# Performance work log

Measured on AMD Instinct MI355X. Metric: run time of the kernel, lower is better.

The kernel has to match this reference:

```python
import jax, jax.numpy as jnp
import numpy as np

DIM = 192
NUM_HEADS = 6
KSZ = 7
MLP_RATIO = 4.0
LEVELS = 8
EPS = 1e-5


def layernorm(x, w, b):
    mu = jnp.mean(x, axis=-1, keepdims=True)
    var = jnp.mean(jnp.square(x - mu), axis=-1, keepdims=True)
    return (x - mu) * jax.lax.rsqrt(var + EPS) * w + b


def na2d(x, qkv_w, qkv_b, proj_w, proj_b, rpb):
    # Neighborhood attention 2D with relative position bias (NATTEN semantics:
    # window of KSZ x KSZ keys per query, clamped to stay inside the image).
    B, H, W, C = x.shape
    nh, hd = NUM_HEADS, C // NUM_HEADS
    scale = hd ** -0.5
    qkv = (x @ qkv_w.T + qkv_b).reshape(B, H, W, 3, nh, hd)
    q = qkv[..., 0, :, :] * scale  # [B,H,W,nh,hd]
    k = qkv[..., 1, :, :]
    v = qkv[..., 2, :, :]

    si = jnp.clip(jnp.arange(H) - KSZ // 2, 0, H - KSZ)
    idx_i = si[:, None] + jnp.arange(KSZ)  # [H,KSZ] row indices of each window
    sj = jnp.clip(jnp.arange(W) - KSZ // 2, 0, W - KSZ)
    idx_j = sj[:, None] + jnp.arange(KSZ)  # [W,KSZ]

    def gather_win(t):  # [B,H,W,nh,hd] -> [B,H,KSZ,W,KSZ,nh,hd]
        t = jnp.take(t, idx_i.reshape(-1), axis=1).reshape(B, H, KSZ, W, nh, hd)
        t = jnp.take(t, idx_j.reshape(-1), axis=3).reshape(B, H, KSZ, W, KSZ, nh, hd)
        return t

    kw = gather_win(k)
    vw = gather_win(v)

    # scores over the KSZ x KSZ neighborhood
    scores = jnp.einsum('bxynd,bxiyjnd->bxynij', q, kw)  # [B,H,W,nh,KSZ,KSZ]

    # relative position bias: rpb is [nh, 2K-1, 2K-1]
    rel_i = idx_i - jnp.arange(H)[:, None] + (KSZ - 1)  # [H,KSZ] in [0,2K-2]
    rel_j = idx_j - jnp.arange(W)[:, None] + (KSZ - 1)  # [W,KSZ]
    bias = rpb[:, rel_i][:, :, :, rel_j]  # [nh,H,KSZ,W,KSZ]
    scores = scores + bias.transpose(1, 3, 0, 2, 4)[None]

    attn = jax.nn.softmax(scores.reshape(B, H, W, nh, KSZ * KSZ), axis=-1)
    attn = attn.reshape(B, H, W, nh, KSZ, KSZ)
    out = jnp.einsum('bxynij,bxiyjnd->bxynd', attn, vw).reshape(B, H, W, C)
    return out @ proj_w.T + proj_b


def setup_inputs() -> dict:
    key = jax.random.key(0)
    ks = jax.random.split(key, 8)
    C = DIM
    hidden = int(C * MLP_RATIO)
    init = lambda k, shape: (jax.random.normal(k, shape, dtype=jnp.float32) * 0.02)
    return {
        'x': jax.random.normal(ks[0], (1, 128, 128, C), dtype=jnp.float32),
        'qkv_w': init(ks[1], (3 * C, C)),
        'qkv_b': jnp.zeros((3 * C,), jnp.float32),
        'proj_w': init(ks[2], (C, C)),
        'proj_b': jnp.zeros((C,), jnp.float32),
        'rpb': init(ks[3], (NUM_HEADS, 2 * KSZ - 1, 2 * KSZ - 1)),
        'ln1_w': jnp.ones((C,), jnp.float32),
        'ln1_b': jnp.zeros((C,), jnp.float32),
        'ln2_w': jnp.ones((C,), jnp.float32),
        'ln2_b': jnp.zeros((C,), jnp.float32),
        'fc1_w': init(ks[4], (hidden, C)),
        'fc1_b': jnp.zeros((hidden,), jnp.float32),
        'fc2_w': init(ks[5], (C, hidden)),
        'fc2_b': jnp.zeros((C,), jnp.float32),
        'gamma1': jnp.ones((LEVELS, C), jnp.float32),
        'gamma2': jnp.ones((LEVELS, C), jnp.float32),
        'quality': 4,
    }


def reference(x, qkv_w, qkv_b, proj_w, proj_b, rpb, ln1_w, ln1_b, ln2_w, ln2_b,
              fc1_w, fc1_b, fc2_w, fc2_b, gamma1, gamma2, quality):
    # eval-mode quality gating; quality is an integer so l = quality % 1 == 0
    s = int(quality) - 1
    g1 = jnp.abs(gamma1[s])
    g2 = jnp.abs(gamma2[s])

    shortcut = x
    h = layernorm(x, ln1_w, ln1_b)
    a = na2d(h, qkv_w, qkv_b, proj_w, proj_b, rpb)
    x = shortcut + g1 * a
    h2 = layernorm(x, ln2_w, ln2_b)
    m = jax.nn.gelu(h2 @ fc1_w.T + fc1_b, approximate=False) @ fc2_w.T + fc2_b
    x = x + g2 * m
    return x
```

## Files before the change

### kernel.cpp

```cpp
#include <hip/hip_runtime.h>
#include <hip/hip_bf16.h>
#include <math.h>

#define DIM 192
#define NHD 6
#define HD 32
#define KSZ 7
#define HID 768
#define IMH 128
#define IMW 128
#define NPIX (IMH*IMW)
#define WIN 14
#define KPAD 40

typedef __attribute__((ext_vector_type(8))) short short8;
typedef __attribute__((ext_vector_type(4))) float f32x4;

__global__ __launch_bounds__(256) void cvt_ln1(
    const float* __restrict__ qw, const float* __restrict__ pw,
    const float* __restrict__ f1, const float* __restrict__ f2,
    __hip_bfloat16* dq, __hip_bfloat16* dp, __hip_bfloat16* df1, __hip_bfloat16* df2,
    const float* __restrict__ x, const float* __restrict__ w, const float* __restrict__ b,
    __hip_bfloat16* __restrict__ hout)
{
    int blk = blockIdx.x, t = threadIdx.x;
    if (blk < 1728) {
        const float* s; __hip_bfloat16* d; int idx;
        if (blk < 432)       { s = qw; d = dq;  idx = blk * 256 + t; }
        else if (blk < 576)  { s = pw; d = dp;  idx = (blk - 432) * 256 + t; }
        else if (blk < 1152) { s = f1; d = df1; idx = (blk - 576) * 256 + t; }
        else                 { s = f2; d = df2; idx = (blk - 1152) * 256 + t; }
        d[idx] = __float2bfloat16(s[idx]);
        return;
    }
    int wid  = ((blk - 1728) * 256 + t) >> 6;
    int lane = t & 63;
    const float* xp = x + (size_t)wid * DIM;
    float v0 = xp[lane], v1 = xp[lane + 64], v2 = xp[lane + 128];
    float s = v0 + v1 + v2;
    #pragma unroll
    for (int off = 32; off > 0; off >>= 1) s += __shfl_down(s, off);
    float mu = __shfl(s, 0) * (1.0f / DIM);
    float d0 = v0 - mu, d1 = v1 - mu, d2 = v2 - mu;
    float q = d0*d0 + d1*d1 + d2*d2;
    #pragma unroll
    for (int off = 32; off > 0; off >>= 1) q += __shfl_down(q, off);
    float rstd = rsqrtf(__shfl(q, 0) * (1.0f / DIM) + 1e-5f);
    __hip_bfloat16* op = hout + (size_t)wid * DIM;
    op[lane]       = __float2bfloat16(d0 * rstd * w[lane]       + b[lane]);
    op[lane + 64]  = __float2bfloat16(d1 * rstd * w[lane + 64]  + b[lane + 64]);
    op[lane + 128] = __float2bfloat16(d2 * rstd * w[lane + 128] + b[lane + 128]);
}

__device__ __forceinline__ void gl_lds16(const void* g, void* l) {
    __builtin_amdgcn_global_load_lds(
        (const __attribute__((address_space(1))) void*)g,
        (__attribute__((address_space(3))) void*)l, 16, 0, 0);
}

template<int mode>
__global__ __launch_bounds__(256) void gemm_k192(
    const __hip_bfloat16* __restrict__ A, const __hip_bfloat16* __restrict__ W,
    const float* __restrict__ bias,
    float* outf, __hip_bfloat16* outb, __hip_bfloat16* kb, __hip_bfloat16* vb, int N)
{
    __shared__ __hip_bfloat16 As[128 * 192];
    __shared__ __hip_bfloat16 Bs[64 * 192];
    int tid = threadIdx.x;
    int wave = tid >> 6, lane = tid & 63;
    int m0 = blockIdx.x * 128, n0 = blockIdx.y * 64;
    int q = lane >> 4, col = lane & 15;
    int wm = (wave >> 1) * 64, wn = (wave & 1) * 32;

    const __hip_bfloat16* Ab = A + (size_t)m0 * 192;
    #pragma unroll
    for (int i = 0; i < 12; i++) {
        int c = i * 256 + tid;
        int r = c / 24, kc = c - r * 24;
        int g = kc ^ (r & 7);
        gl_lds16(Ab + r * 192 + g * 8, (char*)As + (i * 256 + wave * 64) * 16);
    }
    const __hip_bfloat16* Wb = W + (size_t)n0 * 192;
    #pragma unroll
    for (int i = 0; i < 6; i++) {
        int c = i * 256 + tid;
        int r = c / 24, kc = c - r * 24;
        int g = kc ^ (r & 7);
        gl_lds16(Wb + r * 192 + g * 8, (char*)Bs + (i * 256 + wave * 64) * 16);
    }
    __syncthreads();

    f32x4 acc[4][2] = {};
    #pragma unroll
    for (int ks = 0; ks < 6; ks++) {
        short8 af[4], bf[2];
        #pragma unroll
        for (int mi = 0; mi < 4; mi++) {
            int r = wm + mi * 16 + col;
            af[mi] = *(const short8*)&As[r * 192 + (((ks * 4 + q) ^ (r & 7)) * 8)];
        }
        #pragma unroll
        for (int ni = 0; ni < 2; ni++) {
            int r = wn + ni * 16 + col;
            bf[ni] = *(const short8*)&Bs[r * 192 + (((ks * 4 + q) ^ (r & 7)) * 8)];
        }
        #pragma unroll
        for (int mi = 0; mi < 4; mi++)
            #pragma unroll
            for (int ni = 0; ni < 2; ni++)
                acc[mi][ni] = __builtin_amdgcn_mfma_f32_16x16x32_bf16(
                    af[mi], bf[ni], acc[mi][ni], 0, 0, 0);
    }

    #pragma unroll
    for (int mi = 0; mi < 4; mi++) {
        #pragma unroll
        for (int r = 0; r < 4; r++) {
            int m = m0 + wm + mi * 16 + q * 4 + r;
            #pragma unroll
            for (int ni = 0; ni < 2; ni++) {
                int n = n0 + wn + ni * 16 + col;
                float v = acc[mi][ni][r] + bias[n];
                if (mode == 0) {
                    int h18 = n >> 5;
                    int sel = h18 / 6;
                    int head = h18 - sel * 6;
                    size_t idx = ((size_t)head * NPIX + m) * 32 + (n & 31);
                    if (sel == 0)      outf[idx] = v * 0.17677669529663687f;
                    else if (sel == 1) kb[idx] = __float2bfloat16(v);
                    else               vb[idx] = __float2bfloat16(v);
                } else {
                    float u = 0.7978845608f * (v + 0.044715f * v * v * v);
                    float t = 1.f - 2.f / (__expf(2.f * u) + 1.f);
                    v = 0.5f * v * (1.f + t);
                    outb[(size_t)m * N + n] = __float2bfloat16(v);
                }
            }
        }
    }
}

__global__ __launch_bounds__(256) void proj_ln(
    const __hip_bfloat16* __restrict__ A, const __hip_bfloat16* __restrict__ W,
    const float* __restrict__ bias,
    float* outf, __hip_bfloat16* hb, const float* __restrict__ resid,
    const float* __restrict__ gamma, const int* __restrict__ quality,
    const float* __restrict__ lnw, const float* __restrict__ lnb)
{
    __shared__ __hip_bfloat16 As[64 * 192];
    __shared__ __hip_bfloat16 Bs[192 * 192];
    int tid = threadIdx.x;
    int wave = tid >> 6, lane = tid & 63;
    int q = lane >> 4, col = lane & 15;
    int m0 = blockIdx.x * 64;

    const __hip_bfloat16* Ab = A + (size_t)m0 * 192;
    #pragma unroll
    for (int i = 0; i < 6; i++) {
        int c = i * 256 + tid;
        int r = c / 24, kc = c - r * 24;
        int g = kc ^ (r & 7);
        gl_lds16(Ab + r * 192 + g * 8, (char*)As + (i * 256 + wave * 64) * 16);
    }
    #pragma unroll
    for (int i = 0; i < 18; i++) {
        int c = i * 256 + tid;
        int r = c / 24, kc = c - r * 24;
        int g = kc ^ (r & 7);
        gl_lds16(W + r * 192 + g * 8, (char*)Bs + (i * 256 + wave * 64) * 16);
    }
    __syncthreads();

    f32x4 acc[12] = {};
    #pragma unroll
    for (int ks = 0; ks < 6; ks++) {
        int rA = wave * 16 + col;
        short8 af = *(const short8*)&As[rA * 192 + (((ks * 4 + q) ^ (rA & 7)) * 8)];
        #pragma unroll
        for (int f = 0; f < 12; f++) {
            int rB = f * 16 + col;
            short8 bf = *(const short8*)&Bs[rB * 192 + (((ks * 4 + q) ^ (rB & 7)) * 8)];
            acc[f] = __builtin_amdgcn_mfma_f32_16x16x32_bf16(af, bf, acc[f], 0, 0, 0);
        }
    }

    int s = quality[0] - 1;
    float v[12][4];
    #pragma unroll
    for (int f = 0; f < 12; f++) {
        int n = f * 16 + col;
        float bi = bias[n];
        float g = fabsf(gamma[s * DIM + n]);
        #pragma unroll
        for (int r = 0; r < 4; r++) {
            int m = m0 + wave * 16 + q * 4 + r;
            v[f][r] = resid[(size_t)m * DIM + n] + g * (acc[f][r] + bi);
            outf[(size_t)m * DIM + n] = v[f][r];
        }
    }
    float sm[4] = {}, sq[4] = {};
    #pragma unroll
    for (int f = 0; f < 12; f++)
        #pragma unroll
        for (int r = 0; r < 4; r++) { sm[r] += v[f][r]; sq[r] += v[f][r] * v[f][r]; }
    #pragma unroll
    for (int off = 1; off <= 8; off <<= 1) {
        #pragma unroll
        for (int r = 0; r < 4; r++) {
            sm[r] += __shfl_xor(sm[r], off);
            sq[r] += __shfl_xor(sq[r], off);
        }
    }
    float mu[4], rstd[4];
    #pragma unroll
    for (int r = 0; r < 4; r++) {
        mu[r] = sm[r] * (1.0f / DIM);
        float var = sq[r] * (1.0f / DIM) - mu[r] * mu[r];
        rstd[r] = rsqrtf(var + 1e-5f);
    }
    #pragma unroll
    for (int f = 0; f < 12; f++) {
        int n = f * 16 + col;
        float lw = lnw[n], lb = lnb[n];
        #pragma unroll
        for (int r = 0; r < 4; r++) {
            int m = m0 + wave * 16 + q * 4 + r;
            hb[(size_t)m * DIM + n] = __float2bfloat16((v[f][r] - mu[r]) * rstd[r] * lw + lb);
        }
    }
}

__global__ __launch_bounds__(256) void fc2_gemm(
    const __hip_bfloat16* __restrict__ A, const __hip_bfloat16* __restrict__ W,
    const float* __restrict__ bias,
    float* outf, const float* __restrict__ resid,
    const float* __restrict__ gamma, const int* __restrict__ quality)
{
    __shared__ __hip_bfloat16 As[64 * 192];
    __shared__ __hip_bfloat16 Bs[64 * 192];
    int tid = threadIdx.x;
    int wave = tid >> 6, lane = tid & 63;
    int q = lane >> 4, col = lane & 15;
    int m0 = blockIdx.x * 64, n0 = blockIdx.y * 64;
    int wm = (wave >> 1) * 32, wn = (wave & 1) * 32;

    f32x4 acc[2][2] = {};
    for (int k0 = 0; k0 < HID; k0 += 192) {
        #pragma unroll
        for (int i = 0; i < 6; i++) {
            int c = i * 256 + tid;
            int r = c / 24, kc = c - r * 24;
            int g = kc ^ (r & 7);
            gl_lds16(A + (size_t)(m0 + r) * HID + k0 + g * 8,
                     (char*)As + (i * 256 + wave * 64) * 16);
        }
        #pragma unroll
        for (int i = 0; i < 6; i++) {
            int c = i * 256 + tid;
            int r = c / 24, kc = c - r * 24;
            int g = kc ^ (r & 7);
            gl_lds16(W + (size_t)(n0 + r) * HID + k0 + g * 8,
                     (char*)Bs + (i * 256 + wave * 64) * 16);
        }
        __syncthreads();
        #pragma unroll
        for (int ks = 0; ks < 6; ks++) {
            short8 af[2], bf[2];
            #pragma unroll
            for (int mi = 0; mi < 2; mi++) {
                int r = wm + mi * 16 + col;
                af[mi] = *(const short8*)&As[r * 192 + (((ks * 4 + q) ^ (r & 7)) * 8)];
            }
            #pragma unroll
            for (int ni = 0; ni < 2; ni++) {
                int r = wn + ni * 16 + col;
                bf[ni] = *(const short8*)&Bs[r * 192 + (((ks * 4 + q) ^ (r & 7)) * 8)];
            }
            #pragma unroll
            for (int mi = 0; mi < 2; mi++)
                #pragma unroll
                for (int ni = 0; ni < 2; ni++)
                    acc[mi][ni] = __builtin_amdgcn_mfma_f32_16x16x32_bf16(
                        af[mi], bf[ni], acc[mi][ni], 0, 0, 0);
        }
        __syncthreads();
    }

    int s = quality[0] - 1;
    #pragma unroll
    for (int mi = 0; mi < 2; mi++) {
        #pragma unroll
        for (int r = 0; r < 4; r++) {
            int m = m0 + wm + mi * 16 + q * 4 + r;
            #pragma unroll
            for (int ni = 0; ni < 2; ni++) {
                int n = n0 + wn + ni * 16 + col;
                float g = fabsf(gamma[s * DIM + n]);
                outf[(size_t)m * DIM + n] =
                    resid[(size_t)m * DIM + n] + g * (acc[mi][ni][r] + bias[n]);
            }
        }
    }
}

__device__ __forceinline__ void unpack8(const __hip_bfloat16* ptr, float* f) {
    short8 s8 = *(const short8*)ptr;
    union { short8 v; unsigned u[4]; } c; c.v = s8;
    #pragma unroll
    for (int w = 0; w < 4; w++) {
        f[2*w]   = __uint_as_float(c.u[w] << 16);
        f[2*w+1] = __uint_as_float(c.u[w] & 0xffff0000u);
    }
}

__global__ __launch_bounds__(256, 4) void attn_kernel3(
    const float* __restrict__ qbuf, const __hip_bfloat16* __restrict__ kbuf,
    const __hip_bfloat16* __restrict__ vbuf, const float* __restrict__ rpb,
    __hip_bfloat16* __restrict__ out)
{
    __shared__ __hip_bfloat16 Ks[WIN * WIN * KPAD];
    __shared__ __hip_bfloat16 Vs[WIN * WIN * KPAD];
    __shared__ float rpbs[169];

    int head = blockIdx.y;
    int tile = blockIdx.x;
    int ti0 = (tile >> 4) * 8;
    int tj0 = (tile & 15) * 8;
    int wi0 = ti0 - 3; wi0 = wi0 < 0 ? 0 : (wi0 > IMH - WIN ? IMH - WIN : wi0);
    int wj0 = tj0 - 3; wj0 = wj0 < 0 ? 0 : (wj0 > IMW - WIN ? IMW - WIN : wj0);

    int tid = threadIdx.x;
    const size_t hbase = (size_t)head * NPIX;

    for (int c = tid; c < 784; c += 256) {
        int i = c / 56, part = c - i * 56;
        int n = i * WIN + (part >> 2);
        int dp = part & 3;
        size_t goff = (hbase + (size_t)(wi0 + i) * IMW + wj0) * 32 + part * 8;
        short8 kk = *(const short8*)(kbuf + goff);
        short8 vv = *(const short8*)(vbuf + goff);
        *(short8*)&Ks[n * KPAD + dp * 8] = kk;
        *(short8*)&Vs[n * KPAD + dp * 8] = vv;
    }
    if (tid < 169) rpbs[tid] = rpb[head * 169 + tid];

    int p   = tid >> 2;
    int sub = tid & 3;
    int pi = ti0 + (p >> 3), pj = tj0 + (p & 7);
    int si = pi - 3; si = si < 0 ? 0 : (si > IMH - KSZ ? IMH - KSZ : si);
    int sj = pj - 3; sj = sj < 0 ? 0 : (sj > IMW - KSZ ? IMW - KSZ : sj);
    int bi = si - wi0, bj = sj - wj0;

    const float4* qp = (const float4*)(qbuf + (hbase + (size_t)(pi * IMW + pj)) * 32 + sub * 8);
    float4 q0 = qp[0], q1 = qp[1];
    float q[8] = {q0.x, q0.y, q0.z, q0.w, q1.x, q1.y, q1.z, q1.w};

    __syncthreads();

    float m = -1e30f, l = 0.f;
    float acc[8] = {};
    #pragma unroll
    for (int ki = 0; ki < KSZ; ki++) {
        int rbase = (bi + ki) * WIN + bj;
        const float* rb = &rpbs[(si + ki - pi + 6) * 13 + (sj - pj + 6)];
        float s7[KSZ];
        #pragma unroll
        for (int kj = 0; kj < KSZ; kj++) {
            float kf[8];
            unpack8(&Ks[(rbase + kj) * KPAD + sub * 8], kf);
            float d = q[0]*kf[0] + q[1]*kf[1] + q[2]*kf[2] + q[3]*kf[3]
                    + q[4]*kf[4] + q[5]*kf[5] + q[6]*kf[6] + q[7]*kf[7];
            d += __shfl_xor(d, 1);
            d += __shfl_xor(d, 2);
            s7[kj] = d + rb[kj];
        }
        float rmax = s7[0];
        #pragma unroll
        for (int kj = 1; kj < KSZ; kj++) rmax = fmaxf(rmax, s7[kj]);
        float mn = fmaxf(m, rmax);
        float co = __expf(m - mn);
        l *= co;
        #pragma unroll
        for (int e = 0; e < 8; e++) acc[e] *= co;
        #pragma unroll
        for (int kj = 0; kj < KSZ; kj++) {
            float pw = __expf(s7[kj] - mn);
            l += pw;
            float vf[8];
            unpack8(&Vs[(rbase + kj) * KPAD + sub * 8], vf);
            #pragma unroll
            for (int e = 0; e < 8; e++) acc[e] += pw * vf[e];
        }
        m = mn;
    }
    float rl = 1.f / l;
    __hip_bfloat16* op = out + (size_t)(pi * IMW + pj) * DIM + head * HD + sub * 8;
    #pragma unroll
    for (int e = 0; e < 8; e++) op[e] = __float2bfloat16(acc[e] * rl);
}

extern "C" void kernel_launch(void* const* d_in, const int* in_sizes, int n_in,
                              void* d_out, int out_size, void* d_ws, size_t ws_size,
                              hipStream_t stream)
{
    const float* x      = (const float*)d_in[0];
    const float* qkv_w  = (const float*)d_in[1];
    const float* qkv_b  = (const float*)d_in[2];
    const float* proj_w = (const float*)d_in[3];
    const float* proj_b = (const float*)d_in[4];
    const float* rpb    = (const float*)d_in[5];
    const float* ln1_w  = (const float*)d_in[6];
    const float* ln1_b  = (const float*)d_in[7];
    const float* ln2_w  = (const float*)d_in[8];
    const float* ln2_b  = (const float*)d_in[9];
    const float* fc1_w  = (const float*)d_in[10];
    const float* fc1_b  = (const float*)d_in[11];
    const float* fc2_w  = (const float*)d_in[12];
    const float* fc2_b  = (const float*)d_in[13];
    const float* gamma1 = (const float*)d_in[14];
    const float* gamma2 = (const float*)d_in[15];
    const int*   quality= (const int*)d_in[16];
    float* out = (float*)d_out;

    char* ws = (char*)d_ws;
    float*          qbuf   = (float*)ws;
    __hip_bfloat16* kbuf   = (__hip_bfloat16*)(ws + 12582912);
    __hip_bfloat16* vbuf   = (__hip_bfloat16*)(ws + 18874368);
    __hip_bfloat16* m1     = (__hip_bfloat16*)ws;
    __hip_bfloat16* h      = (__hip_bfloat16*)(ws + 37748736);
    __hip_bfloat16* attn_b = (__hip_bfloat16*)(ws + 44040192);
    __hip_bfloat16* wq     = (__hip_bfloat16*)(ws + 50331648);
    __hip_bfloat16* wp     = (__hip_bfloat16*)(ws + 50552832);
    __hip_bfloat16* wf1    = (__hip_bfloat16*)(ws + 50626560);
    __hip_bfloat16* wf2    = (__hip_bfloat16*)(ws + 50921472);

    cvt_ln1<<<1728 + NPIX / 4, 256, 0, stream>>>(
        qkv_w, proj_w, fc1_w, fc2_w, wq, wp, wf1, wf2, x, ln1_w, ln1_b, h);
    gemm_k192<0><<<dim3(NPIX / 128, 9), 256, 0, stream>>>(
        h, wq, qkv_b, qbuf, nullptr, kbuf, vbuf, 576);
    attn_kernel3<<<dim3(256, NHD), 256, 0, stream>>>(qbuf, kbuf, vbuf, rpb, attn_b);
    proj_ln<<<NPIX / 64, 256, 0, stream>>>(
        attn_b, wp, proj_b, out, h, x, gamma1, quality, ln2_w, ln2_b);
    gemm_k192<1><<<dim3(NPIX / 128, 12), 256, 0, stream>>>(
        h, wf1, fc1_b, nullptr, m1, nullptr, nullptr, HID);
    fc2_gemm<<<dim3(NPIX / 64, 3), 256, 0, stream>>>(
        m1, wf2, fc2_b, out, out, gamma2, quality);
}
```

Before: 182.5 us.

## Fuse fc1+GELU and fc2 into one MLP kernel keeping hidden activations in LDS

Replaces the separate fc1 GEMM (writing the 768-wide bf16 hidden tensor to global memory) and the fc2 GEMM with a single kernel. Each 64-row block loops over eight 96-wide hidden chunks: it computes fc1 plus GELU into shared memory, then immediately accumulates the fc2 contribution. fc2 weights are pre-permuted into chunked layout during conversion. This removes the hidden-activation round trip through HBM and one launch, at the cost of large LDS use (~100KB, low occupancy), 256 blocks only, and no overlap of chunk loads with compute.

```diff
diff --git a/kernel.cpp b/kernel.cpp
--- a/kernel.cpp
+++ b/kernel.cpp
@@ -25,12 +25,14 @@
 {
     int blk = blockIdx.x, t = threadIdx.x;
     if (blk < 1728) {
-        const float* s; __hip_bfloat16* d; int idx;
-        if (blk < 432)       { s = qw; d = dq;  idx = blk * 256 + t; }
-        else if (blk < 576)  { s = pw; d = dp;  idx = (blk - 432) * 256 + t; }
-        else if (blk < 1152) { s = f1; d = df1; idx = (blk - 576) * 256 + t; }
-        else                 { s = f2; d = df2; idx = (blk - 1152) * 256 + t; }
-        d[idx] = __float2bfloat16(s[idx]);
+        if (blk < 432)       { int i = blk * 256 + t; dq[i] = __float2bfloat16(qw[i]); }
+        else if (blk < 576)  { int i = (blk - 432) * 256 + t; dp[i] = __float2bfloat16(pw[i]); }
+        else if (blk < 1152) { int i = (blk - 576) * 256 + t; df1[i] = __float2bfloat16(f1[i]); }
+        else {
+            int i = (blk - 1152) * 256 + t;
+            int n = i / 768, k = i - n * 768;
+            df2[(k / 96) * 24576 + n * 128 + (k % 96)] = __float2bfloat16(f2[i]);
+        }
         return;
     }
     int wid  = ((blk - 1728) * 256 + t) >> 6;
@@ -121,20 +123,13 @@
             for (int ni = 0; ni < 2; ni++) {
                 int n = n0 + wn + ni * 16 + col;
                 float v = acc[mi][ni][r] + bias[n];
-                if (mode == 0) {
-                    int h18 = n >> 5;
-                    int sel = h18 / 6;
-                    int head = h18 - sel * 6;
-                    size_t idx = ((size_t)head * NPIX + m) * 32 + (n & 31);
-                    if (sel == 0)      outf[idx] = v * 0.17677669529663687f;
-                    else if (sel == 1) kb[idx] = __float2bfloat16(v);
-                    else               vb[idx] = __float2bfloat16(v);
-                } else {
-                    float u = 0.7978845608f * (v + 0.044715f * v * v * v);
-                    float t = 1.f - 2.f / (__expf(2.f * u) + 1.f);
-                    v = 0.5f * v * (1.f + t);
-                    outb[(size_t)m * N + n] = __float2bfloat16(v);
-                }
+                int h18 = n >> 5;
+                int sel = h18 / 6;
+                int head = h18 - sel * 6;
+                size_t idx = ((size_t)head * NPIX + m) * 32 + (n & 31);
+                if (sel == 0)      outf[idx] = v * 0.17677669529663687f;
+                else if (sel == 1) kb[idx] = __float2bfloat16(v);
+                else               vb[idx] = __float2bfloat16(v);
             }
         }
     }
@@ -230,75 +225,99 @@
     }
 }
 
-__global__ __launch_bounds__(256) void fc2_gemm(
-    const __hip_bfloat16* __restrict__ A, const __hip_bfloat16* __restrict__ W,
-    const float* __restrict__ bias,
-    float* outf, const float* __restrict__ resid,
+__global__ __launch_bounds__(256) void mlp_gemm(
+    const __hip_bfloat16* __restrict__ h2, const __hip_bfloat16* __restrict__ w1,
+    const float* __restrict__ b1, const __hip_bfloat16* __restrict__ w2p,
+    const float* __restrict__ b2, float* __restrict__ out,
     const float* __restrict__ gamma, const int* __restrict__ quality)
 {
-    __shared__ __hip_bfloat16 As[64 * 192];
-    __shared__ __hip_bfloat16 Bs[64 * 192];
+    __shared__ __hip_bfloat16 Hs[64 * 192];
+    __shared__ __hip_bfloat16 W1s[96 * 192];
+    __shared__ __hip_bfloat16 W2s[192 * 128];
+    __shared__ __hip_bfloat16 M1s[4 * 16 * 104];
     int tid = threadIdx.x;
     int wave = tid >> 6, lane = tid & 63;
     int q = lane >> 4, col = lane & 15;
-    int m0 = blockIdx.x * 64, n0 = blockIdx.y * 64;
-    int wm = (wave >> 1) * 32, wn = (wave & 1) * 32;
-
-    f32x4 acc[2][2] = {};
-    for (int k0 = 0; k0 < HID; k0 += 192) {
-        #pragma unroll
-        for (int i = 0; i < 6; i++) {
+    int m0 = blockIdx.x * 64;
+
+    const __hip_bfloat16* Hb = h2 + (size_t)m0 * 192;
+    #pragma unroll
+    for (int i = 0; i < 6; i++) {
+        int c = i * 256 + tid;
+        int r = c / 24, kc = c - r * 24;
+        int g = kc ^ (r & 7);
+        gl_lds16(Hb + r * 192 + g * 8, (char*)Hs + (i * 256 + wave * 64) * 16);
+    }
+
+    f32x4 acc2[12] = {};
+    for (int ch = 0; ch < 8; ch++) {
+        if (ch) __syncthreads();
+        #pragma unroll
+        for (int i = 0; i < 9; i++) {
             int c = i * 256 + tid;
             int r = c / 24, kc = c - r * 24;
             int g = kc ^ (r & 7);
-            gl_lds16(A + (size_t)(m0 + r) * HID + k0 + g * 8,
-                     (char*)As + (i * 256 + wave * 64) * 16);
-        }
-        #pragma unroll
-        for (int i = 0; i < 6; i++) {
+            gl_lds16(w1 + (size_t)(ch * 96 + r) * 192 + g * 8,
+                     (char*)W1s + (i * 256 + wave * 64) * 16);
+        }
+        #pragma unroll
+        for (int i = 0; i < 12; i++) {
             int c = i * 256 + tid;
-            int r = c / 24, kc = c - r * 24;
+            int r = c >> 4, kc = c & 15;
             int g = kc ^ (r & 7);
-            gl_lds16(W + (size_t)(n0 + r) * HID + k0 + g * 8,
-                     (char*)Bs + (i * 256 + wave * 64) * 16);
+            gl_lds16(w2p + (size_t)ch * 24576 + r * 128 + g * 8,
+                     (char*)W2s + (i * 256 + wave * 64) * 16);
         }
         __syncthreads();
+
+        f32x4 acc1[6] = {};
         #pragma unroll
         for (int ks = 0; ks < 6; ks++) {
-            short8 af[2], bf[2];
-            #pragma unroll
-            for (int mi = 0; mi < 2; mi++) {
-                int r = wm + mi * 16 + col;
-                af[mi] = *(const short8*)&As[r * 192 + (((ks * 4 + q) ^ (r & 7)) * 8)];
+            int rA = wave * 16 + col;
+            short8 af = *(const short8*)&Hs[rA * 192 + (((ks * 4 + q) ^ (rA & 7)) * 8)];
+            #pragma unroll
+            for (int f = 0; f < 6; f++) {
+                int rB = f * 16 + col;
+                short8 bf = *(const short8*)&W1s[rB * 192 + (((ks * 4 + q) ^ (rB & 7)) * 8)];
+                acc1[f] = __builtin_amdgcn_mfma_f32_16x16x32_bf16(af, bf, acc1[f], 0, 0, 0);
             }
-            #pragma unroll
-            for (int ni = 0; ni < 2; ni++) {
-                int r = wn + ni * 16 + col;
-                bf[ni] = *(const short8*)&Bs[r * 192 + (((ks * 4 + q) ^ (r & 7)) * 8)];
+        }
+        __hip_bfloat16* mw = &M1s[wave * 16 * 104];
+        #pragma unroll
+        for (int f = 0; f < 6; f++) {
+            float bb = b1[ch * 96 + f * 16 + col];
+            #pragma unroll
+            for (int r = 0; r < 4; r++) {
+                float v = acc1[f][r] + bb;
+                float u = 0.7978845608f * (v + 0.044715f * v * v * v);
+                float t = 1.f - 2.f / (__expf(2.f * u) + 1.f);
+                v = 0.5f * v * (1.f + t);
+                mw[(q * 4 + r) * 104 + f * 16 + col] = __float2bfloat16(v);
             }
-            #pragma unroll
-            for (int mi = 0; mi < 2; mi++)
-                #pragma unroll
-                for (int ni = 0; ni < 2; ni++)
-                    acc[mi][ni] = __builtin_amdgcn_mfma_f32_16x16x32_bf16(
-                        af[mi], bf[ni], acc[mi][ni], 0, 0, 0);
-        }
-        __syncthreads();
+        }
+        #pragma unroll
+        for (int ks = 0; ks < 3; ks++) {
+            short8 af = *(const short8*)&mw[col * 104 + ks * 32 + q * 8];
+            #pragma unroll
+            for (int f = 0; f < 12; f++) {
+                int rB = f * 16 + col;
+                short8 bf = *(const short8*)&W2s[rB * 128 + (((ks * 4 + q) ^ (rB & 7)) * 8)];
+                acc2[f] = __builtin_amdgcn_mfma_f32_16x16x32_bf16(af, bf, acc2[f], 0, 0, 0);
+            }
+        }
     }
 
     int s = quality[0] - 1;
     #pragma unroll
-    for (int mi = 0; mi < 2; mi++) {
+    for (int f = 0; f < 12; f++) {
+        int n = f * 16 + col;
+        float g = fabsf(gamma[s * DIM + n]);
+        float bb = b2[n];
         #pragma unroll
         for (int r = 0; r < 4; r++) {
-            int m = m0 + wm + mi * 16 + q * 4 + r;
-            #pragma unroll
-            for (int ni = 0; ni < 2; ni++) {
-                int n = n0 + wn + ni * 16 + col;
-                float g = fabsf(gamma[s * DIM + n]);
-                outf[(size_t)m * DIM + n] =
-                    resid[(size_t)m * DIM + n] + g * (acc[mi][ni][r] + bias[n]);
-            }
+            int m = m0 + wave * 16 + q * 4 + r;
+            size_t o = (size_t)m * DIM + n;
+            out[o] = out[o] + g * (acc2[f][r] + bb);
         }
     }
 }
@@ -426,23 +445,20 @@
     float*          qbuf   = (float*)ws;
     __hip_bfloat16* kbuf   = (__hip_bfloat16*)(ws + 12582912);
     __hip_bfloat16* vbuf   = (__hip_bfloat16*)(ws + 18874368);
-    __hip_bfloat16* m1     = (__hip_bfloat16*)ws;
     __hip_bfloat16* h      = (__hip_bfloat16*)(ws + 37748736);
     __hip_bfloat16* attn_b = (__hip_bfloat16*)(ws + 44040192);
     __hip_bfloat16* wq     = (__hip_bfloat16*)(ws + 50331648);
     __hip_bfloat16* wp     = (__hip_bfloat16*)(ws + 50552832);
     __hip_bfloat16* wf1    = (__hip_bfloat16*)(ws + 50626560);
-    __hip_bfloat16* wf2    = (__hip_bfloat16*)(ws + 50921472);
+    __hip_bfloat16* wf2p   = (__hip_bfloat16*)(ws + 50921472);
 
     cvt_ln1<<<1728 + NPIX / 4, 256, 0, stream>>>(
-        qkv_w, proj_w, fc1_w, fc2_w, wq, wp, wf1, wf2, x, ln1_w, ln1_b, h);
+        qkv_w, proj_w, fc1_w, fc2_w, wq, wp, wf1, wf2p, x, ln1_w, ln1_b, h);
     gemm_k192<0><<<dim3(NPIX / 128, 9), 256, 0, stream>>>(
         h, wq, qkv_b, qbuf, nullptr, kbuf, vbuf, 576);
     attn_kernel3<<<dim3(256, NHD), 256, 0, stream>>>(qbuf, kbuf, vbuf, rpb, attn_b);
     proj_ln<<<NPIX / 64, 256, 0, stream>>>(
         attn_b, wp, proj_b, out, h, x, gamma1, quality, ln2_w, ln2_b);
-    gemm_k192<1><<<dim3(NPIX / 128, 12), 256, 0, stream>>>(
-        h, wf1, fc1_b, nullptr, m1, nullptr, nullptr, HID);
-    fc2_gemm<<<dim3(NPIX / 64, 3), 256, 0, stream>>>(
-        m1, wf2, fc2_b, out, out, gamma2, quality);
-}
+    mlp_gemm<<<NPIX / 64, 256, 0, stream>>>(
+        h, wf1, fc1_b, wf2p, fc2_b, out, gamma2, quality);
+}
```

Result: slower. 190.8 us (+4.6%).
